# Kernel optimization log

Hardware: AMD Instinct MI355X
Metric: run time of the kernel (lower is better)

The kernel has to match this reference:

```python
import jax, jax.numpy as jnp
import numpy as np

B, HGRID, WGRID = 4, 32, 32
L = 1 + HGRID * WGRID          # cls token + spatial tokens
INPUT_DIM = 512
HEAD_DIM = 512
N_HEAD = 8
QKV_DIM = HEAD_DIM * N_HEAD    # 4096


def pos_embed_2d(h, w, C, dtype):
    """Standard 2D sinusoidal positional embedding, shape (h*w, C)."""
    d = C // 4
    omega = 1.0 / (10000.0 ** (jnp.arange(d, dtype=jnp.float32) / d))
    ey = jnp.arange(h, dtype=jnp.float32)[:, None] * omega      # (h, d)
    ex = jnp.arange(w, dtype=jnp.float32)[:, None] * omega      # (w, d)
    emb_y = jnp.concatenate([jnp.sin(ey), jnp.cos(ey)], -1)     # (h, 2d)
    emb_x = jnp.concatenate([jnp.sin(ex), jnp.cos(ex)], -1)     # (w, 2d)
    emb = jnp.concatenate([
        jnp.broadcast_to(emb_y[:, None, :], (h, w, 2 * d)),
        jnp.broadcast_to(emb_x[None, :, :], (h, w, 2 * d)),
    ], -1)                                                       # (h, w, C)
    return emb.reshape(h * w, C).astype(dtype)


def setup_inputs() -> dict:
    key = jax.random.key(0)
    ks = jax.random.split(key, 16)
    s = 0.02
    inp = {
        "x": jax.random.normal(ks[0], (B, L, INPUT_DIM), dtype=jnp.float32),
        # Q/K/V linear: weight (out, in) as in torch Linear, bias zeros (per _init_bias)
        "Wq": jax.random.normal(ks[1], (QKV_DIM, INPUT_DIM), jnp.float32) * s,
        "bq": jnp.zeros((QKV_DIM,), jnp.float32),
        "Wk": jax.random.normal(ks[2], (QKV_DIM, INPUT_DIM), jnp.float32) * s,
        "bk": jnp.zeros((QKV_DIM,), jnp.float32),
        "Wv": jax.random.normal(ks[3], (QKV_DIM, INPUT_DIM), jnp.float32) * s,
        "bv": jnp.zeros((QKV_DIM,), jnp.float32),
        # 1x1 conv poolers: weight (out_ch, in_ch) = (HEAD_DIM, HEAD_DIM)
        "Wpq": jax.random.normal(ks[4], (HEAD_DIM, HEAD_DIM), jnp.float32) * s,
        "bpq": jax.random.normal(ks[5], (HEAD_DIM,), jnp.float32) * s,
        "Wpk": jax.random.normal(ks[6], (HEAD_DIM, HEAD_DIM), jnp.float32) * s,
        "bpk": jax.random.normal(ks[7], (HEAD_DIM,), jnp.float32) * s,
        "Wpv": jax.random.normal(ks[8], (HEAD_DIM, HEAD_DIM), jnp.float32) * s,
        "bpv": jax.random.normal(ks[9], (HEAD_DIM,), jnp.float32) * s,
        # dispatcher linear: (INPUT_DIM, QKV_DIM)
        "Wd": jax.random.normal(ks[10], (INPUT_DIM, QKV_DIM), jnp.float32) * s,
        "bd": jax.random.normal(ks[11], (INPUT_DIM,), jnp.float32) * s,
        "h": HGRID,
        "w": WGRID,
    }
    return inp


def _pool(t, Wp, bp):
    """AttentionPooler with kernel=1/stride=1: pointwise conv on spatial tokens,
    cls token passed through unchanged. t: (B, n_head, L, head_dim)."""
    cls_tok = t[:, :, :1, :]
    sp = jnp.einsum('bnlc,oc->bnlo', t[:, :, 1:, :], Wp) + bp
    return jnp.concatenate([cls_tok, sp], axis=2)


def reference(x, Wq, bq, Wk, bk, Wv, bv, Wpq, bpq, Wpk, bpk, Wpv, bpv, Wd, bd, h, w):
    Bs, Ls, _ = x.shape

    def proj(Wt, bt):
        y = jnp.einsum('bli,oi->blo', x, Wt) + bt
        return y.reshape(Bs, Ls, N_HEAD, HEAD_DIM).transpose(0, 2, 1, 3)  # (B,nh,L,hd)

    Q = proj(Wq, bq)
    K = proj(Wk, bk)
    V = proj(Wv, bv)

    PQ = _pool(Q, Wpq, bpq)
    PK = _pool(K, Wpk, bpk)
    PV = _pool(V, Wpv, bpv)

    # relative positional encoding added to pooled Q's spatial tokens
    emb = pos_embed_2d(h, w, HEAD_DIM, PQ.dtype)                 # (h*w, hd)
    PQ = jnp.concatenate([PQ[:, :, :1, :], PQ[:, :, 1:, :] + emb], axis=2)

    scale = 1.0 / jnp.sqrt(jnp.asarray(HEAD_DIM, PQ.dtype))
    logits = jnp.einsum('bnqc,bnkc->bnqk', PQ, PK) * scale
    attn = jax.nn.softmax(logits, axis=-1)
    sa = jnp.einsum('bnqk,bnkc->bnqc', attn, PV)

    # skip connection on spatial tokens only (cls row excluded)
    sa = jnp.concatenate([sa[:, :, :1, :], sa[:, :, 1:, :] + Q[:, :, 1:, :]], axis=2)

    stacked = sa.transpose(0, 2, 1, 3).reshape(Bs, Ls, QKV_DIM)
    out = jnp.einsum('blq,oq->blo', stacked, Wd) + bd
    return out
```

## Files before the change

### kernel.cpp

```cpp
#include <hip/hip_runtime.h>


typedef unsigned short u16;
typedef __attribute__((ext_vector_type(8))) short short8;
typedef __attribute__((ext_vector_type(4))) float floatx4;
typedef __attribute__((ext_vector_type(4))) unsigned short us4;

__device__ __forceinline__ u16 f2bf(float f) {
  union { float f; unsigned u; } x; x.f = f;
  unsigned r = (x.u + 0x7fffu + ((x.u >> 16) & 1u)) >> 16;
  return (u16)r;
}
__device__ __forceinline__ float bf2f(u16 u) {
  union { unsigned u; float f; } x; x.u = ((unsigned)u) << 16;
  return x.f;
}

__device__ __forceinline__ void gld_lds16(const void* g, void* l) {
  __builtin_amdgcn_global_load_lds(
      (const __attribute__((address_space(1))) void*)g,
      (__attribute__((address_space(3))) void*)l, 16, 0, 0);
}

struct CvtArgs { const float* src[8]; u16* dst[8]; int n4[8]; };

__global__ __launch_bounds__(256) void cvt_all(CvtArgs a, int total4, float* __restrict__ e) {
  int t = blockIdx.x * 256 + threadIdx.x;
  if (t >= total4) {
    int et = (t - total4) * 4;
    if (et >= 1024 * 512) return;
#pragma unroll
    for (int u = 0; u < 4; ++u) {
      int idx = et + u;
      int c = idx & 511, sp = idx >> 9;
      int y = sp >> 5, xg = sp & 31;
      int j = c & 127, seg = c >> 7;
      float omega = expf(-(float)j * (9.210340371976184f / 128.f));
      float arg = (float)((seg < 2) ? y : xg) * omega;
      e[idx] = (seg & 1) ? cosf(arg) : sinf(arg);
    }
    return;
  }
#pragma unroll
  for (int s = 0; s < 8; ++s) {
    if (t < a.n4[s]) {
      const float* sp = a.src[s] + (long)t * 4;
      u16* dp = a.dst[s] + (long)t * 4;
      float4 v = *(const float4*)sp;
      dp[0] = f2bf(v.x); dp[1] = f2bf(v.y); dp[2] = f2bf(v.z); dp[3] = f2bf(v.w);
      return;
    }
    t -= a.n4[s];
  }
}

struct CF {
  const u16* W;
  const u16* Wp;
  const u16* xb;
  const float *bq, *bk, *bv, *bpq, *bpk, *bpv;
  u16 *PQ, *PK, *PVt;
  float* bc;
};

__global__ __launch_bounds__(256) void cls_fold(CF a) {
  int t = blockIdx.x * 256 + threadIdx.x;
  if (t < 12288) {
    int mat = t >> 12, o2 = t & 4095, n = o2 >> 9, ch = o2 & 511;
    const float* bsrc = (mat == 0) ? a.bq : (mat == 1) ? a.bk : a.bv;
    float ac[4];
    float bias = bsrc[o2];
#pragma unroll
    for (int b = 0; b < 4; ++b) ac[b] = bias;
    const u16* w = a.W + (long)t * 512;
    for (int k8 = 0; k8 < 64; ++k8) {
      short8 wv = *(const short8*)(w + k8 * 8);
      float wf[8];
#pragma unroll
      for (int e = 0; e < 8; ++e) wf[e] = bf2f((u16)wv[e]);
#pragma unroll
      for (int b = 0; b < 4; ++b) {
        short8 xv = *(const short8*)(a.xb + ((long)b * 1025) * 512 + k8 * 8);
#pragma unroll
        for (int e = 0; e < 8; ++e) ac[b] += wf[e] * bf2f((u16)xv[e]);
      }
    }
#pragma unroll
    for (int b = 0; b < 4; ++b) {
      long bn = b * 8 + n;
      u16 v = f2bf(ac[b]);
      if (mat == 0)      a.PQ[(bn * 1025 + 1024) * 512 + ch] = v;
      else if (mat == 1) a.PK[(bn * 1025 + 1024) * 512 + ch] = v;
      else               a.PVt[(bn * 512 + ch) * 1088 + 1024] = v;
    }
  } else {
    int t2 = t - 12288;
    if (t2 >= 12288) return;
    int mat = t2 >> 12, o2 = t2 & 4095, n = o2 >> 9, o = o2 & 511;
    const u16* wp = a.Wp + mat * 262144 + o * 512;
    const float* bsrc = (mat == 0) ? a.bq : (mat == 1) ? a.bk : a.bv;
    const float* bpp = (mat == 0) ? a.bpq : (mat == 1) ? a.bpk : a.bpv;
    float s = bpp[o];
    for (int k8 = 0; k8 < 64; ++k8) {
      short8 wv = *(const short8*)(wp + k8 * 8);
      const float* bb = bsrc + n * 512 + k8 * 8;
#pragma unroll
      for (int e = 0; e < 8; ++e) s += bf2f((u16)wv[e]) * bb[e];
    }
    a.bc[t2] = s;
  }
}

__global__ __launch_bounds__(256) void s_edge(const u16* __restrict__ PQ,
                                              const u16* __restrict__ PK,
                                              u16* __restrict__ S, int nh) {
  int flat = blockIdx.x;
  int head, seg;
  if (nh == 32) {
    int xcd = flat & 7, s = flat >> 3;
    head = xcd + 8 * (s >> 3);
    seg = s & 7;
  } else {
    head = flat >> 3;
    seg = flat & 7;
  }
  const u16* pq = PQ + (long)head * 1025 * 512;
  const u16* pk = PK + (long)head * 1025 * 512;
  u16* sh = S + (long)head * 1025 * 1088;
#pragma unroll
  for (int i = 0; i < 2; ++i) {
    int local = i * 256 + (int)threadIdx.x;
    if (local >= 257) continue;
    int e = seg * 257 + local;
    if (e >= 2049) continue;
    int q, kv;
    if (e < 1025) { q = 1024; kv = e; }
    else { q = e - 1025; kv = 1024; }
    const u16* a = pq + (long)q * 512;
    const u16* b = pk + (long)kv * 512;
    float acc = 0.f;
    for (int k8 = 0; k8 < 64; ++k8) {
      short8 av = *(const short8*)(a + k8 * 8);
      short8 bv = *(const short8*)(b + k8 * 8);
#pragma unroll
      for (int u = 0; u < 8; ++u) acc += bf2f((u16)av[u]) * bf2f((u16)bv[u]);
    }
    sh[(long)q * 1088 + kv] = f2bf(acc * 0.04419417382415922f);
  }
}

__global__ __launch_bounds__(256) void softmax_rows(u16* __restrict__ S) {
  int flat = blockIdx.x;
  int xcd = flat & 7, s0 = flat >> 3;
  int zi = s0 / 257, blk = s0 - zi * 257;
  int head = xcd + 8 * zi;
  int wv = threadIdx.x >> 6, lane = threadIdx.x & 63;
  int row_i = blk * 4 + wv;
  if (row_i > 1024) return;
  u16* row = S + ((long)head * 1025 + row_i) * 1088;
  float v[16];
  float mx = -1e30f;
#pragma unroll
  for (int i = 0; i < 4; ++i) {
    us4 p = *(const us4*)(row + i * 256 + lane * 4);
#pragma unroll
    for (int e = 0; e < 4; ++e) { v[i * 4 + e] = bf2f(p[e]); mx = fmaxf(mx, v[i * 4 + e]); }
  }
  float e1024 = (lane == 0) ? bf2f(row[1024]) : -1e30f;
  mx = fmaxf(mx, e1024);
  for (int o = 32; o > 0; o >>= 1) mx = fmaxf(mx, __shfl_xor(mx, o, 64));
  float s = 0.f;
#pragma unroll
  for (int i = 0; i < 16; ++i) { v[i] = __expf(v[i] - mx); s += v[i]; }
  e1024 = (lane == 0) ? __expf(e1024 - mx) : 0.f;
  s += e1024;
  for (int o = 32; o > 0; o >>= 1) s += __shfl_xor(s, o, 64);
  float inv = 1.0f / s;
#pragma unroll
  for (int i = 0; i < 4; ++i) {
    us4 q;
#pragma unroll
    for (int e = 0; e < 4; ++e) q[e] = f2bf(v[i * 4 + e] * inv);
    *(us4*)(row + i * 256 + lane * 4) = q;
  }
  if (lane < 16) {
    us4 q;
#pragma unroll
    for (int e = 0; e < 4; ++e) q[e] = 0;
    if (lane == 0) q[0] = f2bf(e1024 * inv);
    *(us4*)(row + 1024 + lane * 4) = q;
  }
}

__global__ __launch_bounds__(256) void reduce2(const float* __restrict__ part,
                                               const float* __restrict__ bd,
                                               float* __restrict__ out) {
  int t = blockIdx.x * 256 + threadIdx.x;
  long i = (long)t * 4;
  const long STR = 4100ll * 512;
  float4 a = *(const float4*)(part + i);
  float4 b = *(const float4*)(part + i + STR);
  float4 bb = *(const float4*)(bd + (int)(i & 511));
  float4 r;
  r.x = a.x + b.x + bb.x;
  r.y = a.y + b.y + bb.y;
  r.z = a.z + b.z + bb.z;
  r.w = a.w + b.w + bb.w;
  *(float4*)(out + i) = r;
}

struct GP {
  const u16* A; const u16* A2; const u16* B; const u16* B2;
  const float* c0; const float* c1; const float* c2;
  const float* emb; const u16* resid;
  u16* o0; u16* o1; u16* o2;
  u16* p0; u16* p1; u16* p2;
  float* of; int bz0;
};

template <int MODE>
__global__ __launch_bounds__(256) void gemm_bt(GP g) {
  constexpr int KLEN = (MODE == 5) ? 2048 : ((MODE == 4) ? 1088 : 512);
  constexpr int KITER = KLEN / 64;
  __shared__ u16 smem[16384];
  u16* As = smem;
  u16* Bs = smem + 8192;
  const int tid = threadIdx.x;
  const int lane = tid & 63;
  const int wv = tid >> 6;
  const int wr = wv >> 1, wc = wv & 1;
  const int ccol = lane & 15;
  const int rgrp = lane >> 4;

  int mt, nt, bz, mh = 0;
  if constexpr (MODE == 3 || MODE == 4) {
    constexpr int PER = (MODE == 3) ? 64 : 36;
    constexpr int NTW = (MODE == 3) ? 8 : 4;
    int flat = blockIdx.x;
    int xcd = flat & 7, s = flat >> 3;
    bz = xcd + 8 * (s / PER);
    int tile = s % PER;
    mt = tile / NTW;
    nt = tile % NTW;
  } else if constexpr (MODE == 6) {
    int flat = blockIdx.x;
    mh = flat >> 4;
    int tile = flat & 15;
    mt = tile >> 2; nt = tile & 3; bz = 0;
  } else {
    mt = blockIdx.y; nt = blockIdx.x; bz = blockIdx.z;
  }
  const int gbz = g.bz0 + bz;

  const u16* Ap = g.A;
  const u16* Bp = g.B;
  if constexpr (MODE == 0) {
    if (nt >= 96) Bp = g.B2;
  }

  int a_row[4], b_row[4], kx[4];
#pragma unroll
  for (int c = 0; c < 4; ++c) {
    int idx = c * 256 + tid;
    int row = idx >> 3;
    kx[c] = ((idx & 7) ^ (row & 7)) * 8;
    {
      int r = mt * 128 + row;
      int off;
      if constexpr (MODE == 0) { off = ((r >> 10) * 1025 + 1 + (r & 1023)) * 512; }
      else if constexpr (MODE == 3) { off = gbz * (1025 * 512) + r * 512; }
      else if constexpr (MODE == 4) { r = r < 1024 ? r : 1024; off = bz * (1025 * 1088) + r * 1088; }
      else if constexpr (MODE == 6) { off = (mh >> 3) * 262144 + r * 512; }
      else { r = r < 4099 ? r : 4099; off = r * 4096; }
      a_row[c] = off;
    }
    {
      int off;
      if constexpr (MODE == 6) {
        int rb = idx >> 4, s2 = idx & 15;
        int cg = (s2 - ((rb >> 3) << 1)) & 15;
        off = mh * 262144 + rb * 512 + nt * 128 + cg * 8;
      } else {
        int r = nt * 128 + row;
        if constexpr (MODE == 0) { off = ((nt >= 96) ? (r - 12288) : r) * 512; }
        else if constexpr (MODE == 3) { off = gbz * (1025 * 512) + r * 512; }
        else if constexpr (MODE == 4) { off = gbz * (512 * 1088) + r * 1088; }
        else { off = r * 4096; }
      }
      b_row[c] = off;
    }
  }

  floatx4 acc[4][4];
  {
    float binit[4] = {0.f, 0.f, 0.f, 0.f};
    if constexpr (MODE == 0) {
      int sec = nt >> 5;
      const float* bs = (sec < 3) ? (g.c0 + sec * 4096) : g.c1;
#pragma unroll
      for (int j = 0; j < 4; ++j) binit[j] = bs[(nt & 31) * 128 + wc * 64 + j * 16 + ccol];
    }
#pragma unroll
    for (int i = 0; i < 4; ++i)
#pragma unroll
      for (int j = 0; j < 4; ++j)
#pragma unroll
        for (int rr = 0; rr < 4; ++rr) acc[i][j][rr] = binit[j];
  }

  const int kbase = (MODE == 5) ? bz * 2048 : 0;
  const int l15 = lane & 15;
  const int lq = lane >> 4;
  const int l7 = lane & 7;

  for (int kt = 0; kt < KITER; ++kt) {
    const int k0 = kbase + kt * 64;
#pragma unroll
    for (int c = 0; c < 4; ++c)
      gld_lds16(Ap + a_row[c] + k0 + kx[c], (char*)As + (c * 256 + wv * 64) * 16);
#pragma unroll
    for (int c = 0; c < 4; ++c) {
      if constexpr (MODE == 6)
        gld_lds16(Bp + b_row[c] + k0 * 512, (char*)Bs + (c * 256 + wv * 64) * 16);
      else
        gld_lds16(Bp + b_row[c] + k0 + kx[c], (char*)Bs + (c * 256 + wv * 64) * 16);
    }
    __syncthreads();
#pragma unroll
    for (int ks = 0; ks < 2; ++ks) {
      const int ch = ((ks * 4 + lq) ^ l7) * 8;
      short8 af[4], bfr[4];
#pragma unroll
      for (int i = 0; i < 4; ++i)
        af[i] = *(const short8*)(As + (wr * 64 + i * 16 + l15) * 64 + ch);
      if constexpr (MODE == 6) {
#pragma unroll
        for (int j = 0; j < 4; ++j) {
          int ro = ((wc * 64 + j * 16 + l15) + ((ks * 4 + lq) << 4)) & 127;
          const u16* bp2 = Bs + (ks * 32 + lq * 8) * 128 + ro;
          short8 tv;
#pragma unroll
          for (int e = 0; e < 8; ++e) tv[e] = (short)bp2[e * 128];
          bfr[j] = tv;
        }
      } else {
#pragma unroll
        for (int j = 0; j < 4; ++j)
          bfr[j] = *(const short8*)(Bs + (wc * 64 + j * 16 + l15) * 64 + ch);
      }
#pragma unroll
      for (int i = 0; i < 4; ++i)
#pragma unroll
        for (int j = 0; j < 4; ++j)
          acc[i][j] = __builtin_amdgcn_mfma_f32_16x16x32_bf16(af[i], bfr[j], acc[i][j], 0, 0, 0);
    }
    __syncthreads();
  }

  if constexpr (MODE == 0) {
    const int sec = nt >> 5;
    if (sec == 2) {
#pragma unroll
      for (int i = 0; i < 4; ++i)
#pragma unroll
        for (int j = 0; j < 4; ++j)
#pragma unroll
          for (int rr = 0; rr < 4; ++rr) {
            int lr2 = wc * 64 + j * 16 + ccol;
            int lc2 = wr * 64 + i * 16 + rgrp * 4 + rr;
            smem[lr2 * 128 + (lc2 ^ ((lr2 & 15) << 3))] = f2bf(acc[i][j][rr]);
          }
      __syncthreads();
      {
        int b = mt >> 3, sp0 = (mt & 7) * 128;
        int nt2 = nt & 31, n = nt2 >> 2, ch0 = (nt2 & 3) * 128;
        long bn = b * 8 + n;
#pragma unroll
        for (int q = 0; q < 8; ++q) {
          int cid = q * 256 + tid;
          int r = cid >> 4;
          int c = cid & 15;
          int pc = c ^ (r & 15);
          short8 val = *(const short8*)(smem + r * 128 + pc * 8);
          *(short8*)(g.p2 + (bn * 512 + ch0 + r) * 1088 + sp0 + c * 8) = val;
        }
      }
    } else {
#pragma unroll
      for (int i = 0; i < 4; ++i)
#pragma unroll
        for (int j = 0; j < 4; ++j)
#pragma unroll
          for (int rr = 0; rr < 4; ++rr) {
            int lr = wr * 64 + i * 16 + rgrp * 4 + rr;
            int lc = wc * 64 + j * 16 + ccol;
            smem[lr * 128 + (lc ^ (rgrp << 4))] = f2bf(acc[i][j][rr]);
          }
      __syncthreads();
#pragma unroll
      for (int q = 0; q < 8; ++q) {
        int cid = q * 256 + tid;
        int r = cid >> 4;
        int c = cid & 15;
        int pc = c ^ ((((unsigned)r >> 2) & 3) << 1);
        short8 val = *(const short8*)(smem + r * 128 + pc * 8);
        int grow = mt * 128 + r;
        int b = grow >> 10, sp = grow & 1023;
        int gcol = (nt & 31) * 128 + c * 8;
        int n = gcol >> 9, ch2 = gcol & 511;
        long bn = b * 8 + n;
        if (sec == 0) {
          const float* ep = g.emb + sp * 512 + ch2;
          float4 e0 = *(const float4*)ep;
          float4 e1 = *(const float4*)(ep + 4);
          float ee[8] = {e0.x, e0.y, e0.z, e0.w, e1.x, e1.y, e1.z, e1.w};
          short8 outv;
#pragma unroll
          for (int e = 0; e < 8; ++e) outv[e] = (short)f2bf(bf2f((u16)val[e]) + ee[e]);
          *(short8*)(g.o0 + (bn * 1025 + sp) * 512 + ch2) = outv;
        } else if (sec == 1) {
          *(short8*)(g.o1 + (bn * 1025 + sp) * 512 + ch2) = val;
        } else {
          *(short8*)(g.o2 + (bn * 1025 + 1 + sp) * 512 + ch2) = val;
        }
      }
    }
  } else if constexpr (MODE == 3 || MODE == 4 || MODE == 6) {
#pragma unroll
    for (int i = 0; i < 4; ++i)
#pragma unroll
      for (int j = 0; j < 4; ++j)
#pragma unroll
        for (int rr = 0; rr < 4; ++rr) {
          int lr = wr * 64 + i * 16 + rgrp * 4 + rr;
          int lc = wc * 64 + j * 16 + ccol;
          float v = acc[i][j][rr];
          if constexpr (MODE == 3) v *= 0.04419417382415922f;
          smem[lr * 128 + (lc ^ (rgrp << 4))] = f2bf(v);
        }
    __syncthreads();
#pragma unroll
    for (int q = 0; q < 8; ++q) {
      int cid = q * 256 + tid;
      int r = cid >> 4;
      int c = cid & 15;
      int pc = c ^ ((((unsigned)r >> 2) & 3) << 1);
      short8 val = *(const short8*)(smem + r * 128 + pc * 8);
      int grow = mt * 128 + r;
      if constexpr (MODE == 3) {
        *(short8*)(g.o0 + ((long)bz * 1025 + grow) * 1088 + nt * 128 + c * 8) = val;
      } else if constexpr (MODE == 6) {
        *(short8*)(g.o0 + ((long)(mh * 512) + grow) * 512 + nt * 128 + c * 8) = val;
      } else {
        if (grow <= 1024) {
          int gcol0 = nt * 128 + c * 8;
          short8 outv = val;
          int l = (grow == 1024) ? 0 : grow + 1;
          if (grow < 1024) {
            short8 rs = *(const short8*)(g.resid + ((long)gbz * 1025 + l) * 512 + gcol0);
#pragma unroll
            for (int e = 0; e < 8; ++e)
              outv[e] = (short)f2bf(bf2f((u16)val[e]) + bf2f((u16)rs[e]));
          }
          int b = gbz >> 3, n = gbz & 7;
          *(short8*)(g.o0 + (((long)b * 1025 + l) * 8 + n) * 512 + gcol0) = outv;
        }
      }
    }
  } else {
#pragma unroll
    for (int i = 0; i < 4; ++i) {
#pragma unroll
      for (int j = 0; j < 4; ++j) {
        const int gcol = nt * 128 + wc * 64 + j * 16 + ccol;
#pragma unroll
        for (int rr = 0; rr < 4; ++rr) {
          const int grow = mt * 128 + wr * 64 + i * 16 + rgrp * 4 + rr;
          if (grow < 4100)
            g.of[((long)bz * 4100 + grow) * 512 + gcol] = acc[i][j][rr];
        }
      }
    }
  }
}

extern "C" void kernel_launch(void* const* d_in, const int* in_sizes, int n_in,
                              void* d_out, int out_size, void* d_ws, size_t ws_size,
                              hipStream_t stream) {
  const float* x   = (const float*)d_in[0];
  const float* Wq  = (const float*)d_in[1];
  const float* bq  = (const float*)d_in[2];
  const float* Wk  = (const float*)d_in[3];
  const float* bk  = (const float*)d_in[4];
  const float* Wv  = (const float*)d_in[5];
  const float* bv  = (const float*)d_in[6];
  const float* Wpq = (const float*)d_in[7];
  const float* bpq = (const float*)d_in[8];
  const float* Wpk = (const float*)d_in[9];
  const float* bpk = (const float*)d_in[10];
  const float* Wpv = (const float*)d_in[11];
  const float* bpv = (const float*)d_in[12];
  const float* Wd  = (const float*)d_in[13];
  const float* bd  = (const float*)d_in[14];
  float* out = (float*)d_out;

  char* ws = (char*)d_ws;
  size_t off = 0;
  auto alloc = [&](size_t bytes) {
    char* p = ws + off;
    off += (bytes + 255) & ~(size_t)255;
    return p;
  };
  u16* Wpqb = (u16*)alloc(512ull * 512 * 2);
  u16* Wpkb = (u16*)alloc(512ull * 512 * 2);
  u16* Wpvb = (u16*)alloc(512ull * 512 * 2);
  u16* Wdb  = (u16*)alloc(4096ull * 512 * 2);
  u16* Q    = (u16*)alloc(32ull * 1025 * 512 * 2);
  u16* PQ   = (u16*)alloc(32ull * 1025 * 512 * 2);
  u16* PK   = (u16*)alloc(32ull * 1025 * 512 * 2);
  u16* PVt  = (u16*)alloc(32ull * 512 * 1088 * 2);
  size_t s_off = off;
  u16* xb   = (u16*)alloc(4100ull * 512 * 2);
  u16* Wqb  = (u16*)alloc(4096ull * 512 * 2);
  u16* Wkb  = (u16*)alloc(4096ull * 512 * 2);
  u16* Wvb  = (u16*)alloc(4096ull * 512 * 2);
  u16* Wc   = (u16*)alloc(3ull * 4096 * 512 * 2);
  float* bc = (float*)alloc(3ull * 4096 * 4);
  float* embp = (float*)alloc(1024ull * 512 * 4);
  size_t fixed_need = off;
  u16* S = (u16*)(ws + s_off);
  float* part = (float*)PQ;
  (void)in_sizes; (void)n_in; (void)out_size; (void)Wkb; (void)Wvb;
  (void)Wpkb; (void)Wpvb;

  const size_t sbytes = 1025ull * 1088 * 2;
  size_t need1 = s_off + 32ull * sbytes;
  size_t need2 = s_off + 16ull * sbytes;
  size_t stk4_off = s_off + ((8ull * sbytes + 255) & ~(size_t)255);
  size_t need4 = stk4_off + 4100ull * 4096 * 2;
  int nchunk;
  u16* stk;
  if (ws_size >= need1)      { nchunk = 1; stk = PK; }
  else if (ws_size >= need2 && ws_size >= fixed_need) { nchunk = 2; stk = PK; }
  else if (ws_size >= need4 && ws_size >= fixed_need) {
    nchunk = 4; stk = (u16*)(ws + stk4_off);
  } else return;
  if (nchunk == 2) {
    size_t stk2_off = s_off + ((16ull * sbytes + 255) & ~(size_t)255);
    if (ws_size >= stk2_off + 4100ull * 4096 * 2) stk = (u16*)(ws + stk2_off);
    else {
      nchunk = 4;
      if (ws_size >= need4) stk = (u16*)(ws + stk4_off);
      else return;
    }
  }
  int hpc = 32 / nchunk;

  CvtArgs ca;
  ca.src[0] = x;   ca.dst[0] = xb;   ca.n4[0] = 4100 * 512 / 4;
  ca.src[1] = Wq;  ca.dst[1] = Wqb;  ca.n4[1] = 4096 * 512 / 4;
  ca.src[2] = Wk;  ca.dst[2] = Wkb;  ca.n4[2] = 4096 * 512 / 4;
  ca.src[3] = Wv;  ca.dst[3] = Wvb;  ca.n4[3] = 4096 * 512 / 4;
  ca.src[4] = Wpq; ca.dst[4] = Wpqb; ca.n4[4] = 512 * 512 / 4;
  ca.src[5] = Wpk; ca.dst[5] = Wpkb; ca.n4[5] = 512 * 512 / 4;
  ca.src[6] = Wpv; ca.dst[6] = Wpvb; ca.n4[6] = 512 * 512 / 4;
  ca.src[7] = Wd;  ca.dst[7] = Wdb;  ca.n4[7] = 512 * 4096 / 4;
  int total4 = 0;
  for (int s = 0; s < 8; ++s) total4 += ca.n4[s];
  int grid1 = (total4 + 1024 * 512 / 4 + 255) / 256;
  cvt_all<<<grid1, 256, 0, stream>>>(ca, total4, embp);

  {
    GP g = {};
    g.A = Wpqb; g.B = Wqb; g.o0 = Wc;
    gemm_bt<6><<<dim3(384, 1, 1), 256, 0, stream>>>(g);
  }
  {
    CF cf;
    cf.W = Wqb; cf.Wp = Wpqb; cf.xb = xb;
    cf.bq = bq; cf.bk = bk; cf.bv = bv;
    cf.bpq = bpq; cf.bpk = bpk; cf.bpv = bpv;
    cf.PQ = PQ; cf.PK = PK; cf.PVt = PVt; cf.bc = bc;
    cls_fold<<<96, 256, 0, stream>>>(cf);
  }

  {
    GP g = {};
    g.A = xb; g.B = Wc; g.B2 = Wqb;
    g.c0 = bc; g.c1 = bq; g.emb = embp;
    g.o0 = PQ; g.o1 = PK; g.o2 = Q; g.p2 = PVt;
    gemm_bt<0><<<dim3(128, 32, 1), 256, 0, stream>>>(g);
  }

  for (int c = 0; c < nchunk; ++c) {
    GP g3 = {}; g3.A = PQ; g3.B = PK; g3.o0 = S; g3.bz0 = c * hpc;
    gemm_bt<3><<<dim3(64 * hpc, 1, 1), 256, 0, stream>>>(g3);
    s_edge<<<hpc * 8, 256, 0, stream>>>(
        PQ + (long)c * hpc * 1025 * 512, PK + (long)c * hpc * 1025 * 512, S, hpc);
    softmax_rows<<<257 * hpc, 256, 0, stream>>>(S);
    GP g4 = {}; g4.A = S; g4.B = PVt; g4.resid = Q; g4.o0 = stk; g4.bz0 = c * hpc;
    gemm_bt<4><<<dim3(36 * hpc, 1, 1), 256, 0, stream>>>(g4);
  }

  {
    GP g = {}; g.A = stk; g.B = Wdb; g.of = part;
    gemm_bt<5><<<dim3(4, 33, 2), 256, 0, stream>>>(g);
  }
  reduce2<<<(4100 * 512 / 4 + 255) / 256, 256, 0, stream>>>(part, bd, out);
}
```

Measured before the change: 464.2 us.

## Parallelize cls_fold per-wave and split V-projection into separate XCD-mapped GEMM

cls_fold now assigns one wavefront per output dot product, with lanes splitting the K dimension and a shuffle reduction at the end, instead of one thread looping over all 512 inputs. The grid grows from 96 to 6144 blocks, which should remove a long serial tail. The V-section of the fused projection GEMM moves into a new MODE 2 launch that uses an XCD-aware tile mapping and writes the transposed PVt output, so the main GEMM only handles the Q/K/skip sections. This adds a kernel launch but removes a branch on the section inside the main GEMM epilogue.

```diff
diff --git a/kernel.cpp b/kernel.cpp
--- a/kernel.cpp
+++ b/kernel.cpp
@@ -64,50 +64,55 @@
 };
 
 __global__ __launch_bounds__(256) void cls_fold(CF a) {
-  int t = blockIdx.x * 256 + threadIdx.x;
-  if (t < 12288) {
-    int mat = t >> 12, o2 = t & 4095, n = o2 >> 9, ch = o2 & 511;
+  int wid = blockIdx.x * 4 + (threadIdx.x >> 6);
+  int lane = threadIdx.x & 63;
+  if (wid < 12288) {
+    int mat = wid >> 12, o2 = wid & 4095, n = o2 >> 9, ch = o2 & 511;
+    short8 wv = *(const short8*)(a.W + (long)wid * 512 + lane * 8);
+    float wf[8];
+#pragma unroll
+    for (int e = 0; e < 8; ++e) wf[e] = bf2f((u16)wv[e]);
+    float ac[4] = {0.f, 0.f, 0.f, 0.f};
+#pragma unroll
+    for (int b = 0; b < 4; ++b) {
+      short8 xv = *(const short8*)(a.xb + ((long)b * 1025) * 512 + lane * 8);
+#pragma unroll
+      for (int e = 0; e < 8; ++e) ac[b] += wf[e] * bf2f((u16)xv[e]);
+    }
+#pragma unroll
+    for (int o = 32; o > 0; o >>= 1)
+#pragma unroll
+      for (int b = 0; b < 4; ++b) ac[b] += __shfl_xor(ac[b], o, 64);
+    if (lane == 0) {
+      const float* bsrc = (mat == 0) ? a.bq : (mat == 1) ? a.bk : a.bv;
+      float bias = bsrc[o2];
+#pragma unroll
+      for (int b = 0; b < 4; ++b) {
+        long bn = b * 8 + n;
+        u16 v = f2bf(ac[b] + bias);
+        if (mat == 0)      a.PQ[(bn * 1025 + 1024) * 512 + ch] = v;
+        else if (mat == 1) a.PK[(bn * 1025 + 1024) * 512 + ch] = v;
+        else               a.PVt[(bn * 512 + ch) * 1088 + 1024] = v;
+      }
+    }
+  } else {
+    int t2 = wid - 12288;
+    int mat = t2 >> 12, o2 = t2 & 4095, n = o2 >> 9, o = o2 & 511;
     const float* bsrc = (mat == 0) ? a.bq : (mat == 1) ? a.bk : a.bv;
-    float ac[4];
-    float bias = bsrc[o2];
-#pragma unroll
-    for (int b = 0; b < 4; ++b) ac[b] = bias;
-    const u16* w = a.W + (long)t * 512;
-    for (int k8 = 0; k8 < 64; ++k8) {
-      short8 wv = *(const short8*)(w + k8 * 8);
-      float wf[8];
-#pragma unroll
-      for (int e = 0; e < 8; ++e) wf[e] = bf2f((u16)wv[e]);
-#pragma unroll
-      for (int b = 0; b < 4; ++b) {
-        short8 xv = *(const short8*)(a.xb + ((long)b * 1025) * 512 + k8 * 8);
-#pragma unroll
-        for (int e = 0; e < 8; ++e) ac[b] += wf[e] * bf2f((u16)xv[e]);
-      }
-    }
-#pragma unroll
-    for (int b = 0; b < 4; ++b) {
-      long bn = b * 8 + n;
-      u16 v = f2bf(ac[b]);
-      if (mat == 0)      a.PQ[(bn * 1025 + 1024) * 512 + ch] = v;
-      else if (mat == 1) a.PK[(bn * 1025 + 1024) * 512 + ch] = v;
-      else               a.PVt[(bn * 512 + ch) * 1088 + 1024] = v;
-    }
-  } else {
-    int t2 = t - 12288;
-    if (t2 >= 12288) return;
-    int mat = t2 >> 12, o2 = t2 & 4095, n = o2 >> 9, o = o2 & 511;
-    const u16* wp = a.Wp + mat * 262144 + o * 512;
-    const float* bsrc = (mat == 0) ? a.bq : (mat == 1) ? a.bk : a.bv;
-    const float* bpp = (mat == 0) ? a.bpq : (mat == 1) ? a.bpk : a.bpv;
-    float s = bpp[o];
-    for (int k8 = 0; k8 < 64; ++k8) {
-      short8 wv = *(const short8*)(wp + k8 * 8);
-      const float* bb = bsrc + n * 512 + k8 * 8;
-#pragma unroll
-      for (int e = 0; e < 8; ++e) s += bf2f((u16)wv[e]) * bb[e];
-    }
-    a.bc[t2] = s;
+    short8 wp = *(const short8*)(a.Wp + (long)mat * 262144 + o * 512 + lane * 8);
+    const float* bb = bsrc + n * 512 + lane * 8;
+    float4 b0 = *(const float4*)bb;
+    float4 b1 = *(const float4*)(bb + 4);
+    float bf8[8] = {b0.x, b0.y, b0.z, b0.w, b1.x, b1.y, b1.z, b1.w};
+    float s = 0.f;
+#pragma unroll
+    for (int e = 0; e < 8; ++e) s += bf2f((u16)wp[e]) * bf8[e];
+#pragma unroll
+    for (int o1 = 32; o1 > 0; o1 >>= 1) s += __shfl_xor(s, o1, 64);
+    if (lane == 0) {
+      const float* bpp = (mat == 0) ? a.bpq : (mat == 1) ? a.bpk : a.bpv;
+      a.bc[t2] = s + bpp[o];
+    }
   }
 }
 
@@ -242,6 +247,12 @@
     int tile = s % PER;
     mt = tile / NTW;
     nt = tile % NTW;
+  } else if constexpr (MODE == 2) {
+    int flat = blockIdx.x;
+    int xcd = flat & 7, s = flat >> 3;
+    bz = 0;
+    mt = xcd * 4 + (s >> 5);
+    nt = s & 31;
   } else if constexpr (MODE == 6) {
     int flat = blockIdx.x;
     mh = flat >> 4;
@@ -255,7 +266,7 @@
   const u16* Ap = g.A;
   const u16* Bp = g.B;
   if constexpr (MODE == 0) {
-    if (nt >= 96) Bp = g.B2;
+    if (nt >= 64) Bp = g.B2;
   }
 
   int a_row[4], b_row[4], kx[4];
@@ -267,7 +278,7 @@
     {
       int r = mt * 128 + row;
       int off;
-      if constexpr (MODE == 0) { off = ((r >> 10) * 1025 + 1 + (r & 1023)) * 512; }
+      if constexpr (MODE == 0 || MODE == 2) { off = ((r >> 10) * 1025 + 1 + (r & 1023)) * 512; }
       else if constexpr (MODE == 3) { off = gbz * (1025 * 512) + r * 512; }
       else if constexpr (MODE == 4) { r = r < 1024 ? r : 1024; off = bz * (1025 * 1088) + r * 1088; }
       else if constexpr (MODE == 6) { off = (mh >> 3) * 262144 + r * 512; }
@@ -282,10 +293,11 @@
         off = mh * 262144 + rb * 512 + nt * 128 + cg * 8;
       } else {
         int r = nt * 128 + row;
-        if constexpr (MODE == 0) { off = ((nt >= 96) ? (r - 12288) : r) * 512; }
+        if constexpr (MODE == 0) { off = ((nt >= 64) ? (r - 8192) : r) * 512; }
         else if constexpr (MODE == 3) { off = gbz * (1025 * 512) + r * 512; }
         else if constexpr (MODE == 4) { off = gbz * (512 * 1088) + r * 1088; }
-        else { off = r * 4096; }
+        else if constexpr (MODE == 5) { off = r * 4096; }
+        else { off = r * 512; }
       }
       b_row[c] = off;
     }
@@ -296,9 +308,13 @@
     float binit[4] = {0.f, 0.f, 0.f, 0.f};
     if constexpr (MODE == 0) {
       int sec = nt >> 5;
-      const float* bs = (sec < 3) ? (g.c0 + sec * 4096) : g.c1;
+      const float* bs = (sec < 2) ? (g.c0 + sec * 4096) : g.c1;
 #pragma unroll
       for (int j = 0; j < 4; ++j) binit[j] = bs[(nt & 31) * 128 + wc * 64 + j * 16 + ccol];
+    }
+    if constexpr (MODE == 2) {
+#pragma unroll
+      for (int j = 0; j < 4; ++j) binit[j] = g.c0[nt * 128 + wc * 64 + j * 16 + ccol];
     }
 #pragma unroll
     for (int i = 0; i < 4; ++i)
@@ -357,54 +373,56 @@
     __syncthreads();
   }
 
-  if constexpr (MODE == 0) {
-    const int sec = nt >> 5;
-    if (sec == 2) {
-#pragma unroll
-      for (int i = 0; i < 4; ++i)
-#pragma unroll
-        for (int j = 0; j < 4; ++j)
-#pragma unroll
-          for (int rr = 0; rr < 4; ++rr) {
-            int lr2 = wc * 64 + j * 16 + ccol;
-            int lc2 = wr * 64 + i * 16 + rgrp * 4 + rr;
-            smem[lr2 * 128 + (lc2 ^ ((lr2 & 15) << 3))] = f2bf(acc[i][j][rr]);
-          }
-      __syncthreads();
-      {
-        int b = mt >> 3, sp0 = (mt & 7) * 128;
-        int nt2 = nt & 31, n = nt2 >> 2, ch0 = (nt2 & 3) * 128;
-        long bn = b * 8 + n;
-#pragma unroll
-        for (int q = 0; q < 8; ++q) {
-          int cid = q * 256 + tid;
-          int r = cid >> 4;
-          int c = cid & 15;
-          int pc = c ^ (r & 15);
-          short8 val = *(const short8*)(smem + r * 128 + pc * 8);
-          *(short8*)(g.p2 + (bn * 512 + ch0 + r) * 1088 + sp0 + c * 8) = val;
+  if constexpr (MODE == 2) {
+#pragma unroll
+    for (int i = 0; i < 4; ++i)
+#pragma unroll
+      for (int j = 0; j < 4; ++j)
+#pragma unroll
+        for (int rr = 0; rr < 4; ++rr) {
+          int lr2 = wc * 64 + j * 16 + ccol;
+          int lc2 = wr * 64 + i * 16 + rgrp * 4 + rr;
+          smem[lr2 * 128 + (lc2 ^ ((lr2 & 15) << 3))] = f2bf(acc[i][j][rr]);
         }
-      }
-    } else {
-#pragma unroll
-      for (int i = 0; i < 4; ++i)
-#pragma unroll
-        for (int j = 0; j < 4; ++j)
-#pragma unroll
-          for (int rr = 0; rr < 4; ++rr) {
-            int lr = wr * 64 + i * 16 + rgrp * 4 + rr;
-            int lc = wc * 64 + j * 16 + ccol;
-            smem[lr * 128 + (lc ^ (rgrp << 4))] = f2bf(acc[i][j][rr]);
-          }
-      __syncthreads();
+    __syncthreads();
+    {
+      int b = mt >> 3, sp0 = (mt & 7) * 128;
+      int n = nt >> 2, ch0 = (nt & 3) * 128;
+      long bn = b * 8 + n;
 #pragma unroll
       for (int q = 0; q < 8; ++q) {
         int cid = q * 256 + tid;
         int r = cid >> 4;
         int c = cid & 15;
-        int pc = c ^ ((((unsigned)r >> 2) & 3) << 1);
+        int pc = c ^ (r & 15);
         short8 val = *(const short8*)(smem + r * 128 + pc * 8);
-        int grow = mt * 128 + r;
+        *(short8*)(g.o0 + (bn * 512 + ch0 + r) * 1088 + sp0 + c * 8) = val;
+      }
+    }
+  } else if constexpr (MODE == 0 || MODE == 3 || MODE == 4 || MODE == 6) {
+#pragma unroll
+    for (int i = 0; i < 4; ++i)
+#pragma unroll
+      for (int j = 0; j < 4; ++j)
+#pragma unroll
+        for (int rr = 0; rr < 4; ++rr) {
+          int lr = wr * 64 + i * 16 + rgrp * 4 + rr;
+          int lc = wc * 64 + j * 16 + ccol;
+          float v = acc[i][j][rr];
+          if constexpr (MODE == 3) v *= 0.04419417382415922f;
+          smem[lr * 128 + (lc ^ (rgrp << 4))] = f2bf(v);
+        }
+    __syncthreads();
+#pragma unroll
+    for (int q = 0; q < 8; ++q) {
+      int cid = q * 256 + tid;
+      int r = cid >> 4;
+      int c = cid & 15;
+      int pc = c ^ ((((unsigned)r >> 2) & 3) << 1);
+      short8 val = *(const short8*)(smem + r * 128 + pc * 8);
+      int grow = mt * 128 + r;
+      if constexpr (MODE == 0) {
+        const int sec = nt >> 5;
         int b = grow >> 10, sp = grow & 1023;
         int gcol = (nt & 31) * 128 + c * 8;
         int n = gcol >> 9, ch2 = gcol & 511;
@@ -423,31 +441,7 @@
         } else {
           *(short8*)(g.o2 + (bn * 1025 + 1 + sp) * 512 + ch2) = val;
         }
-      }
-    }
-  } else if constexpr (MODE == 3 || MODE == 4 || MODE == 6) {
-#pragma unroll
-    for (int i = 0; i < 4; ++i)
-#pragma unroll
-      for (int j = 0; j < 4; ++j)
-#pragma unroll
-        for (int rr = 0; rr < 4; ++rr) {
-          int lr = wr * 64 + i * 16 + rgrp * 4 + rr;
-          int lc = wc * 64 + j * 16 + ccol;
-          float v = acc[i][j][rr];
-          if constexpr (MODE == 3) v *= 0.04419417382415922f;
-          smem[lr * 128 + (lc ^ (rgrp << 4))] = f2bf(v);
-        }
-    __syncthreads();
-#pragma unroll
-    for (int q = 0; q < 8; ++q) {
-      int cid = q * 256 + tid;
-      int r = cid >> 4;
-      int c = cid & 15;
-      int pc = c ^ ((((unsigned)r >> 2) & 3) << 1);
-      short8 val = *(const short8*)(smem + r * 128 + pc * 8);
-      int grow = mt * 128 + r;
-      if constexpr (MODE == 3) {
+      } else if constexpr (MODE == 3) {
         *(short8*)(g.o0 + ((long)bz * 1025 + grow) * 1088 + nt * 128 + c * 8) = val;
       } else if constexpr (MODE == 6) {
         *(short8*)(g.o0 + ((long)(mh * 512) + grow) * 512 + nt * 128 + c * 8) = val;
@@ -581,15 +575,20 @@
     cf.bq = bq; cf.bk = bk; cf.bv = bv;
     cf.bpq = bpq; cf.bpk = bpk; cf.bpv = bpv;
     cf.PQ = PQ; cf.PK = PK; cf.PVt = PVt; cf.bc = bc;
-    cls_fold<<<96, 256, 0, stream>>>(cf);
+    cls_fold<<<6144, 256, 0, stream>>>(cf);
   }
 
   {
     GP g = {};
     g.A = xb; g.B = Wc; g.B2 = Wqb;
     g.c0 = bc; g.c1 = bq; g.emb = embp;
-    g.o0 = PQ; g.o1 = PK; g.o2 = Q; g.p2 = PVt;
-    gemm_bt<0><<<dim3(128, 32, 1), 256, 0, stream>>>(g);
+    g.o0 = PQ; g.o1 = PK; g.o2 = Q;
+    gemm_bt<0><<<dim3(96, 32, 1), 256, 0, stream>>>(g);
+  }
+  {
+    GP g = {};
+    g.A = xb; g.B = Wc + 8192 * 512; g.c0 = bc + 8192; g.o0 = PVt;
+    gemm_bt<2><<<dim3(1024, 1, 1), 256, 0, stream>>>(g);
   }
 
   for (int c = 0; c < nchunk; ++c) {
```

After: 429.1 us, median of 2. 1.08x faster.
